# Kernel optimization log

Hardware: AMD Instinct MI355X
Metric: run time of the kernel (lower is better)

Reference implementation:

```python
import jax, jax.numpy as jnp
import numpy as np
from jax import lax

B = 128
NODES = 304
T_STEPS = 20
HID = 64
GCN_IN = 20
N = B * NODES            # 38912 graph nodes
E = N * 16               # 622592 edges
BN_EPS = 1e-5


def setup_inputs() -> dict:
    key = jax.random.key(0)
    ks = jax.random.split(key, 32)
    rn = lambda k, s, sc=0.1: jax.random.normal(k, s, jnp.float32) * sc
    return {
        "data_x": jax.random.normal(ks[0], (N, GCN_IN), jnp.float32),
        "edge_index": jax.random.randint(ks[1], (2, E), 0, N),
        "edge_weight": jax.random.uniform(ks[2], (E,), jnp.float32),
        "tc1_w1": rn(ks[3], (HID, 1, 1, 3)), "tc1_b1": rn(ks[4], (HID,)),
        "tc1_w2": rn(ks[5], (HID, 1, 1, 3)), "tc1_b2": rn(ks[6], (HID,)),
        "tc1_w3": rn(ks[7], (HID, 1, 1, 3)), "tc1_b3": rn(ks[8], (HID,)),
        "gcn_W0": rn(ks[9], (GCN_IN, HID)), "gcn_b0": rn(ks[10], (HID,)),
        "bn0_g": jax.random.uniform(ks[11], (HID,), jnp.float32, 0.5, 1.5), "bn0_b": rn(ks[12], (HID,)),
        "gcn_W1": rn(ks[13], (HID, HID)), "gcn_b1": rn(ks[14], (HID,)),
        "bn1_g": jax.random.uniform(ks[15], (HID,), jnp.float32, 0.5, 1.5), "bn1_b": rn(ks[16], (HID,)),
        "tc2_w1": rn(ks[17], (1, HID, 1, 3)), "tc2_b1": rn(ks[18], (1,)),
        "tc2_w2": rn(ks[19], (1, HID, 1, 3)), "tc2_b2": rn(ks[20], (1,)),
        "tc2_w3": rn(ks[21], (1, HID, 1, 3)), "tc2_b3": rn(ks[22], (1,)),
        "bn2d_g": jax.random.uniform(ks[23], (NODES,), jnp.float32, 0.5, 1.5), "bn2d_b": rn(ks[24], (NODES,)),
        "fc_W": rn(ks[25], (21 * NODES, 2048), 0.01), "fc_b": rn(ks[26], (2048,)),
        "fc4_W": rn(ks[27], (2048, 300), 0.01), "fc4_b": rn(ks[28], (300,)),
    }


def _bn(x, g, b):
    # eval-mode BatchNorm with fresh running stats (mean=0, var=1)
    return x * (g / jnp.sqrt(1.0 + BN_EPS)) + b


def _temporal_conv(X, w1, b1, w2, b2, w3, b3):
    # X: [B, T, nodes, C] -> permute to NCHW [B, C, nodes, T]
    Xp = jnp.transpose(X, (0, 3, 2, 1))
    conv = lambda w, b: lax.conv_general_dilated(
        Xp, w, (1, 1), [(0, 0), (1, 1)],
        dimension_numbers=("NCHW", "OIHW", "NCHW")) + b[None, :, None, None]
    P = conv(w1, b1)
    Q = jax.nn.sigmoid(conv(w2, b2))
    H = jax.nn.relu(P * Q + conv(w3, b3))
    return jnp.transpose(H, (0, 3, 2, 1))  # back to [B, T, nodes, C_out]


def reference(data_x, edge_index, edge_weight,
              tc1_w1, tc1_b1, tc1_w2, tc1_b2, tc1_w3, tc1_b3,
              gcn_W0, gcn_b0, bn0_g, bn0_b,
              gcn_W1, gcn_b1, bn1_g, bn1_b,
              tc2_w1, tc2_b1, tc2_w2, tc2_b2, tc2_w3, tc2_b3,
              bn2d_g, bn2d_b, fc_W, fc_b, fc4_W, fc4_b):
    n = data_x.shape[0]
    b = n // NODES

    # ---- GCN norm (sym, self-loops w=1) ----
    row, col = edge_index[0], edge_index[1]
    loop = jnp.arange(n)
    rowF = jnp.concatenate([row, loop])
    colF = jnp.concatenate([col, loop])
    ewF = jnp.concatenate([edge_weight, jnp.ones((n,), data_x.dtype)])
    deg = jax.ops.segment_sum(ewF, colF, num_segments=n)
    dinv = lax.rsqrt(jnp.maximum(deg, 1e-12))
    norm = dinv[rowF] * ewF * dinv[colF]

    def gconv(x, W, bias):
        h = x @ W
        return jax.ops.segment_sum(h[rowF] * norm[:, None], colF, num_segments=n) + bias

    x = jax.nn.relu(_bn(gconv(data_x, gcn_W0, gcn_b0), bn0_g, bn0_b))
    x = jax.nn.relu(_bn(gconv(x, gcn_W1, gcn_b1), bn1_g, bn1_b))  # [N, HID]

    # ---- temporal conv 1 ----
    X = data_x.reshape(b, T_STEPS, NODES, 1)
    T0 = _temporal_conv(X, tc1_w1, tc1_b1, tc1_w2, tc1_b2, tc1_w3, tc1_b3)  # [B,20,304,HID]

    # gcn_feature.permute(1,0).reshape(-1, 1, nodes, HID)
    gfeat = x.T.reshape(b, 1, NODES, HID)

    T = jnp.concatenate([jax.nn.relu(T0), gfeat], axis=1)  # [B, 21, 304, HID]
    T = jax.nn.relu(T)

    # ---- temporal conv 2 ----
    T = _temporal_conv(T, tc2_w1, tc2_b1, tc2_w2, tc2_b2, tc2_w3, tc2_b3)  # [B,21,304,1]

    # BatchNorm2d over node channel (axis=2 here), eval-mode running stats
    T = T * (bn2d_g / jnp.sqrt(1.0 + BN_EPS))[None, None, :, None] + bn2d_b[None, None, :, None]

    T = T.reshape(b, -1)  # [B, 6384]
    T = jax.nn.relu(T @ fc_W + fc_b)
    return T @ fc4_W + fc4_b  # [B, 300]
```

## Files before the change

### kernel.cpp

```cpp
#include <hip/hip_runtime.h>

#define NODES   304
#define BATCH   128
#define TSTEPS  20
#define HID     64
#define GCNIN   20
#define NN      (BATCH*NODES)
#define NE      (NN*16)
#define SEGSZ   (NN/4)
#define BCAP    64
#define FC1_IN  (21*NODES)
#define KP1     6400
#define FC1_OUT 2048
#define FC2_OUT 300
#define NP2     304
#define BN_EPS  1e-5f

typedef __attribute__((ext_vector_type(8))) short short8;
typedef __attribute__((ext_vector_type(4))) float f32x4;
typedef __attribute__((ext_vector_type(2))) float f32x2;

static __device__ __forceinline__ short f2bf(float x) {
    unsigned u = __float_as_uint(x);
    unsigned r = (u + 0x7FFF + ((u >> 16) & 1)) >> 16;
    return (short)r;
}
static __device__ __forceinline__ float bf2f(unsigned short v) {
    return __uint_as_float((unsigned)v << 16);
}

static __device__ __forceinline__ float fast_sigmoid(float q) {
    return __builtin_amdgcn_rcpf(1.f + __expf(-q));
}

static __device__ __forceinline__ f32x2 pk_fma(f32x2 a, f32x2 b, f32x2 c) {
    f32x2 d;
    asm("v_pk_fma_f32 %0, %1, %2, %3" : "=v"(d) : "v"(a), "v"(b), "v"(c));
    return d;
}

template <int C>
static __device__ __forceinline__ float dppadd(float v) {
    return v + __int_as_float(
        __builtin_amdgcn_update_dpp(0, __float_as_int(v), C, 0xF, 0xF, false));
}
static __device__ __forceinline__ float rsum16(float v) {
    v = dppadd<0x128>(v);
    v = dppadd<0x124>(v);
    v = dppadd<0x122>(v);
    v = dppadd<0x121>(v);
    return v;
}

__global__ void k_bucket(const int* __restrict__ ei, const float* __restrict__ ew,
                         int* __restrict__ cnt, int2* __restrict__ bucket) {
    int e = blockIdx.x * blockDim.x + threadIdx.x;
    if (e < NE) {
        int c = ei[NE + e];
        int slot = atomicAdd(&cnt[c], 1);
        if (slot < BCAP) {
            int2 v;
            v.x = ei[e];
            v.y = __float_as_int(ew[e]);
            bucket[((size_t)c << 6) + slot] = v;
        }
    }
}

__global__ __launch_bounds__(256) void k_cvtX(const float* __restrict__ X,
                                              const int* __restrict__ cnt,
                                              const int2* __restrict__ bucket,
                                              unsigned short* __restrict__ Xb,
                                              float* __restrict__ dinv) {
    int wv = threadIdx.x >> 5, f = threadIdx.x & 31;
    int n = blockIdx.x * 8 + wv;
    __shared__ float rs[8][2];

    int2 e0 = bucket[((size_t)n << 6) + f];
    int2 e1 = bucket[((size_t)n << 6) + 32 + f];
    int deg = cnt[n];
    float xv = (f < GCNIN) ? X[(size_t)n * GCNIN + f] : 0.f;

    int dcap = deg < BCAP ? deg : BCAP;
    float s = ((f < dcap) ? __int_as_float(e0.y) : 0.f) +
              ((32 + f < dcap) ? __int_as_float(e1.y) : 0.f);
    s = rsum16(s);
    if ((f & 15) == 0) rs[wv][f >> 4] = s;
    __syncthreads();

    float dv = rsqrtf(fmaxf(1.f + rs[wv][0] + rs[wv][1], 1e-12f));
    if (f == 0) dinv[n] = dv;
    Xb[(size_t)n * 32 + f] = (f < GCNIN) ? (unsigned short)f2bf(xv * dv)
                                         : (unsigned short)0;
}

static __device__ __forceinline__ void stage_partition(
    int deg, int2 e, int f, int wv, int (*sIdx)[BCAP], float (*sWt)[BCAP],
    int& dcap) {
    dcap = deg < BCAP ? deg : BCAP;
    bool valid = f < dcap;
    int row = e.x;
    float w = __int_as_float(e.y);
    int q = (row >= SEGSZ) + (row >= 2 * SEGSZ) + (row >= 3 * SEGSZ);
    unsigned long long b0 = __ballot(valid && q == 0);
    unsigned long long b1 = __ballot(valid && q == 1);
    unsigned long long b2 = __ballot(valid && q == 2);
    unsigned long long b3 = __ballot(valid && q == 3);
    unsigned long long lmask = (1ULL << f) - 1;
    int pos = 0;
    if (q > 0) pos += __popcll(b0);
    if (q > 1) pos += __popcll(b1);
    if (q > 2) pos += __popcll(b2);
    unsigned long long mybal = (q == 0) ? b0 : (q == 1) ? b1 : (q == 2) ? b2 : b3;
    pos += __popcll(mybal & lmask);
    if (valid) {
        sIdx[wv][pos] = row;
        sWt[wv][pos] = w;
    }
}

__global__ __launch_bounds__(256) void k_gather20(const int* __restrict__ cnt,
                                                  const int2* __restrict__ bucket,
                                                  const float* __restrict__ dinv,
                                                  const unsigned short* __restrict__ Xb,
                                                  const float* __restrict__ W0,
                                                  const float* __restrict__ gb,
                                                  const float* __restrict__ bng,
                                                  const float* __restrict__ bnb,
                                                  const float* __restrict__ W1,
                                                  unsigned short* __restrict__ H1) {
    int wv = threadIdx.x >> 6, f = threadIdx.x & 63;
    int c = blockIdx.x * 4 + wv;
    int g = f >> 4, r = f & 15;
    __shared__ int sIdx[4][BCAP];
    __shared__ float sWt[4][BCAP];
    __shared__ float agg[4][32];
    __shared__ float xs[4][HID];

    int2 be = bucket[((size_t)c << 6) + f];
    int deg = cnt[c];
    float dc = dinv[c];
    unsigned selfv = *(const unsigned*)(Xb + (size_t)c * 32 + 2 * r);

    int dcap;
    stage_partition(deg, be, f, wv, sIdx, sWt, dcap);
    __syncthreads();

    f32x2 acc2;
    acc2[0] = 0.f;
    acc2[1] = 0.f;
    for (int base = 0; base < dcap; base += 16) {
        int idx[4];
        float w[4];
#pragma unroll
        for (int i = 0; i < 4; i++) {
            int l = base + (i << 2) + g;
            int lc = (l < dcap) ? l : dcap - 1;
            idx[i] = sIdx[wv][lc];
            w[i] = (l < dcap) ? sWt[wv][lc] : 0.f;
        }
        unsigned vv[4];
#pragma unroll
        for (int i = 0; i < 4; i++)
            vv[i] = *(const unsigned*)(Xb + (size_t)idx[i] * 32 + 2 * r);
#pragma unroll
        for (int i = 0; i < 4; i++) {
            acc2[0] = fmaf(bf2f((unsigned short)(vv[i] & 0xffff)), w[i], acc2[0]);
            acc2[1] = fmaf(bf2f((unsigned short)(vv[i] >> 16)), w[i], acc2[1]);
        }
    }
    acc2[0] += __shfl_xor(acc2[0], 16);
    acc2[0] += __shfl_xor(acc2[0], 32);
    acc2[1] += __shfl_xor(acc2[1], 16);
    acc2[1] += __shfl_xor(acc2[1], 32);
    if (g == 0) {
        agg[wv][2 * r] = acc2[0] + bf2f((unsigned short)(selfv & 0xffff));
        agg[wv][2 * r + 1] = acc2[1] + bf2f((unsigned short)(selfv >> 16));
    }
    __syncthreads();

    float v = 0.f;
#pragma unroll
    for (int k = 0; k < GCNIN; k++) v = fmaf(agg[wv][k], W0[k * HID + f], v);
    float scale = bng[f] * rsqrtf(1.f + BN_EPS);
    float y = fmaxf(fmaf(v * dc + gb[f], scale, bnb[f]), 0.f);

    xs[wv][f] = y;
    __syncthreads();
    float h = 0.f;
#pragma unroll
    for (int k4 = 0; k4 < HID / 4; k4++) {
        float4 xv = *(const float4*)&xs[wv][k4 * 4];
        h = fmaf(xv.x, W1[(k4 * 4 + 0) * HID + f], h);
        h = fmaf(xv.y, W1[(k4 * 4 + 1) * HID + f], h);
        h = fmaf(xv.z, W1[(k4 * 4 + 2) * HID + f], h);
        h = fmaf(xv.w, W1[(k4 * 4 + 3) * HID + f], h);
    }
    H1[(size_t)c * HID + f] = (unsigned short)f2bf(h * dc);
}

__global__ __launch_bounds__(256) void k_gatherB(const int* __restrict__ cnt,
                                                 const int2* __restrict__ bucket,
                                                 const float* __restrict__ dinv,
                                                 const unsigned short* __restrict__ H,
                                                 const float* __restrict__ gb,
                                                 const float* __restrict__ bng,
                                                 const float* __restrict__ bnb,
                                                 float* __restrict__ XO) {
    int wv = threadIdx.x >> 6, f = threadIdx.x & 63;
    int c = blockIdx.x * 4 + wv;
    int g = f >> 4, r = f & 15;
    __shared__ int sIdx[4][BCAP];
    __shared__ float sWt[4][BCAP];

    int2 be = bucket[((size_t)c << 6) + f];
    int deg = cnt[c];
    float dc = dinv[c];
    ushort4 selfv = *(const ushort4*)(H + (size_t)c * HID + 4 * r);

    int dcap;
    stage_partition(deg, be, f, wv, sIdx, sWt, dcap);
    __syncthreads();

    float a0 = 0.f, a1 = 0.f, a2 = 0.f, a3 = 0.f;
    for (int base = 0; base < dcap; base += 16) {
        int idx[4];
        float w[4];
#pragma unroll
        for (int i = 0; i < 4; i++) {
            int l = base + (i << 2) + g;
            int lc = (l < dcap) ? l : dcap - 1;
            idx[i] = sIdx[wv][lc];
            w[i] = (l < dcap) ? sWt[wv][lc] : 0.f;
        }
        ushort4 hv[4];
#pragma unroll
        for (int i = 0; i < 4; i++)
            hv[i] = *(const ushort4*)(H + (size_t)idx[i] * HID + 4 * r);
#pragma unroll
        for (int i = 0; i < 4; i++) {
            a0 = fmaf(bf2f(hv[i].x), w[i], a0);
            a1 = fmaf(bf2f(hv[i].y), w[i], a1);
            a2 = fmaf(bf2f(hv[i].z), w[i], a2);
            a3 = fmaf(bf2f(hv[i].w), w[i], a3);
        }
    }
    a0 += __shfl_xor(a0, 16); a0 += __shfl_xor(a0, 32);
    a1 += __shfl_xor(a1, 16); a1 += __shfl_xor(a1, 32);
    a2 += __shfl_xor(a2, 16); a2 += __shfl_xor(a2, 32);
    a3 += __shfl_xor(a3, 16); a3 += __shfl_xor(a3, 32);

    if (g == 0) {
        float4 scv = *(const float4*)&bng[4 * r];
        float4 bbv = *(const float4*)&bnb[4 * r];
        float4 gbv = *(const float4*)&gb[4 * r];
        float rr = rsqrtf(1.f + BN_EPS);
        float4 o;
        o.x = fmaxf(fmaf((a0 + bf2f(selfv.x)) * dc + gbv.x, scv.x * rr, bbv.x), 0.f);
        o.y = fmaxf(fmaf((a1 + bf2f(selfv.y)) * dc + gbv.y, scv.y * rr, bbv.y), 0.f);
        o.z = fmaxf(fmaf((a2 + bf2f(selfv.z)) * dc + gbv.z, scv.z * rr, bbv.z), 0.f);
        o.w = fmaxf(fmaf((a3 + bf2f(selfv.w)) * dc + gbv.w, scv.w * rr, bbv.w), 0.f);
        *(float4*)(XO + (size_t)c * HID + 4 * r) = o;
    }
}

__global__ __launch_bounds__(256) void k_xpose(const float* __restrict__ x2,
                                               float* __restrict__ x2t) {
    __shared__ float tile[64][65];
    int n0 = blockIdx.x * 64;
    for (int i = threadIdx.x; i < 4096; i += 256) {
        int r = i >> 6, h = i & 63;
        tile[r][h] = x2[(size_t)(n0 + r) * 64 + h];
    }
    __syncthreads();
    for (int i = threadIdx.x; i < 4096; i += 256) {
        int h = i >> 6, c = i & 63;
        x2t[(size_t)h * NN + n0 + c] = tile[c][h];
    }
}

static __device__ __forceinline__ void load12(const float* base, f32x2 P[2][3]) {
    float4 f0 = *(const float4*)(base);
    float4 f1 = *(const float4*)(base + 4);
    float4 f2 = *(const float4*)(base + 8);
    P[0][0][0] = f0.x; P[0][0][1] = f0.w;
    P[0][1][0] = f0.y; P[0][1][1] = f1.x;
    P[0][2][0] = f0.z; P[0][2][1] = f1.y;
    P[1][0][0] = f1.z; P[1][0][1] = f2.y;
    P[1][1][0] = f1.w; P[1][1][1] = f2.z;
    P[1][2][0] = f2.x; P[1][2][1] = f2.w;
}

__global__ __launch_bounds__(256) void k_temporal2(
    const float* __restrict__ data_x, const float* __restrict__ x2t,
    const float* __restrict__ w1, const float* __restrict__ b1,
    const float* __restrict__ w2, const float* __restrict__ b2,
    const float* __restrict__ w3, const float* __restrict__ b3,
    const float* __restrict__ v1, const float* __restrict__ vb1,
    const float* __restrict__ v2, const float* __restrict__ vb2,
    const float* __restrict__ v3, const float* __restrict__ vb3,
    const float* __restrict__ bn2g, const float* __restrict__ bn2b,
    short* __restrict__ Ab) {
    int bn0 = blockIdx.x * 16;
    int b = bn0 / NODES, node0 = bn0 % NODES;
    int tid = threadIdx.x;
    int p = tid >> 4;
    int c0 = (tid & 15) << 2;
    int node = node0 + p;

    __shared__ float xs[16][22];
    __shared__ float wlds[1344];

    if (tid < 192) {
        wlds[tid] = w1[tid];
        wlds[192 + tid] = w2[tid];
        wlds[384 + tid] = w3[tid];
        wlds[576 + tid] = v1[tid];
        wlds[768 + tid] = v2[tid];
        wlds[960 + tid] = v3[tid];
    }
    if (tid < 64) {
        wlds[1152 + tid] = b1[tid];
        wlds[1216 + tid] = b2[tid];
        wlds[1280 + tid] = b3[tid];
    }
    for (int i = tid; i < 320; i += 256) {
        int t = i >> 4, pp = i & 15;
        xs[pp][t + 1] = data_x[b * (TSTEPS * NODES) + t * NODES + node0 + pp];
    }
    if (tid < 16) { xs[tid][0] = 0.f; xs[tid][21] = 0.f; }

    float cb1 = vb1[0], cb2 = vb2[0], cb3 = vb3[0];
    float s2 = bn2g[node] * rsqrtf(1.f + BN_EPS);
    float bb2 = bn2b[node];
    short* dst = Ab + (size_t)b * KP1;

    __syncthreads();

    f32x2 A1p[2][3], A2p[2][3], A3p[2][3], B1p[2], B2p[2], B3p[2];
    f32x2 U1p[2][3], U2p[2][3], U3p[2][3];
    load12(&wlds[0 + c0 * 3], A1p);
    load12(&wlds[192 + c0 * 3], A2p);
    load12(&wlds[384 + c0 * 3], A3p);
    load12(&wlds[576 + c0 * 3], U1p);
    load12(&wlds[768 + c0 * 3], U2p);
    load12(&wlds[960 + c0 * 3], U3p);
    {
        float4 t1 = *(const float4*)&wlds[1152 + c0];
        float4 t2 = *(const float4*)&wlds[1216 + c0];
        float4 t3 = *(const float4*)&wlds[1280 + c0];
        B1p[0][0] = t1.x; B1p[0][1] = t1.y; B1p[1][0] = t1.z; B1p[1][1] = t1.w;
        B2p[0][0] = t2.x; B2p[0][1] = t2.y; B2p[1][0] = t2.z; B2p[1][1] = t2.w;
        B3p[0][0] = t3.x; B3p[0][1] = t3.y; B3p[1][0] = t3.z; B3p[1][1] = t3.w;
    }

    f32x2 hA2[2] = {}, hB2[2] = {}, hC2[2];
    float xr0 = xs[p][0], xr1 = xs[p][1];

#pragma unroll
    for (int j = 0; j <= 21; j++) {
        if (j < 20) {
            float xr2 = xs[p][j + 2];
            f32x2 x0d, x1d, x2d;
            x0d[0] = xr0; x0d[1] = xr0;
            x1d[0] = xr1; x1d[1] = xr1;
            x2d[0] = xr2; x2d[1] = xr2;
#pragma unroll
            for (int cp = 0; cp < 2; cp++) {
                f32x2 pv = pk_fma(A1p[cp][2], x2d,
                            pk_fma(A1p[cp][1], x1d, pk_fma(A1p[cp][0], x0d, B1p[cp])));
                f32x2 qv = pk_fma(A2p[cp][2], x2d,
                            pk_fma(A2p[cp][1], x1d, pk_fma(A2p[cp][0], x0d, B2p[cp])));
                f32x2 rv = pk_fma(A3p[cp][2], x2d,
                            pk_fma(A3p[cp][1], x1d, pk_fma(A3p[cp][0], x0d, B3p[cp])));
                hC2[cp][0] = fmaxf(fmaf(pv[0], fast_sigmoid(qv[0]), rv[0]), 0.f);
                hC2[cp][1] = fmaxf(fmaf(pv[1], fast_sigmoid(qv[1]), rv[1]), 0.f);
            }
            xr0 = xr1;
            xr1 = xr2;
        } else if (j == 20) {
            const float4 gv = *(const float4*)(x2t + (size_t)(b >> 1) * NN +
                                               (b & 1) * (NODES * HID) + node * HID + c0);
            hC2[0][0] = fmaxf(gv.x, 0.f);
            hC2[0][1] = fmaxf(gv.y, 0.f);
            hC2[1][0] = fmaxf(gv.z, 0.f);
            hC2[1][1] = fmaxf(gv.w, 0.f);
        } else {
            hC2[0][0] = 0.f; hC2[0][1] = 0.f;
            hC2[1][0] = 0.f; hC2[1][1] = 0.f;
        }
        if (j >= 1) {
            int w = j - 1;
            f32x2 pa, qa, ra;
            pa[0] = 0.f; pa[1] = 0.f;
            qa[0] = 0.f; qa[1] = 0.f;
            ra[0] = 0.f; ra[1] = 0.f;
#pragma unroll
            for (int cp = 0; cp < 2; cp++) {
                pa = pk_fma(U1p[cp][0], hA2[cp], pa);
                pa = pk_fma(U1p[cp][1], hB2[cp], pa);
                pa = pk_fma(U1p[cp][2], hC2[cp], pa);
                qa = pk_fma(U2p[cp][0], hA2[cp], qa);
                qa = pk_fma(U2p[cp][1], hB2[cp], qa);
                qa = pk_fma(U2p[cp][2], hC2[cp], qa);
                ra = pk_fma(U3p[cp][0], hA2[cp], ra);
                ra = pk_fma(U3p[cp][1], hB2[cp], ra);
                ra = pk_fma(U3p[cp][2], hC2[cp], ra);
            }
            float pp_ = rsum16(pa[0] + pa[1]);
            float qq_ = rsum16(qa[0] + qa[1]);
            float rr_ = rsum16(ra[0] + ra[1]);
            float P = pp_ + cb1, Q = qq_ + cb2, R = rr_ + cb3;
            float hv = fmaxf(fmaf(P, fast_sigmoid(Q), R), 0.f);
            if ((tid & 15) == 0) dst[w * NODES + node] = f2bf(fmaf(hv, s2, bb2));
        }
        hA2[0] = hB2[0]; hA2[1] = hB2[1];
        hB2[0] = hC2[0]; hB2[1] = hC2[1];
    }
}

__global__ __launch_bounds__(256) void k_cvtW4(const float* __restrict__ W,
                                               short* __restrict__ Wt) {
    __shared__ float t[32][33];
    int tx = threadIdx.x & 31, ty = threadIdx.x >> 5;
    int n0 = blockIdx.x * 32, k0 = blockIdx.y * 32;
#pragma unroll
    for (int r = 0; r < 32; r += 8) {
        int k = k0 + r + ty, n = n0 + tx;
        t[r + ty][tx] = (n < FC2_OUT) ? W[(size_t)k * FC2_OUT + n] : 0.f;
    }
    __syncthreads();
#pragma unroll
    for (int r = 0; r < 32; r += 8) {
        int n = n0 + r + ty;
        if (n < NP2) Wt[(size_t)n * FC1_OUT + k0 + tx] = f2bf(t[tx][r + ty]);
    }
}

#define KSPL1 8
#define KCH1  (KP1 / KSPL1)
__global__ __launch_bounds__(256) void k_gemm1f(const short* __restrict__ Ab,
                                                const float* __restrict__ fcW,
                                                float* __restrict__ part) {
    int lane = threadIdx.x & 63, wv = threadIdx.x >> 6;
    int r = lane & 15, kg = lane >> 4;
    int nb = blockIdx.x * 64, sp = blockIdx.y;

    f32x4 acc[2][4] = {};
    const short* a0 = Ab + (size_t)(wv * 32 + r) * KP1;
    const short* a1 = a0 + (size_t)16 * KP1;

    int k0 = sp * KCH1 + kg * 8;
    const float* wp = fcW + (size_t)k0 * FC1_OUT + nb + r;
    bool tailblk = (sp == KSPL1 - 1);

#pragma unroll 1
    for (int s = 0; s < KCH1 / 32; s++, k0 += 32) {
        short8 av0 = *(const short8*)(a0 + k0);
        short8 av1 = *(const short8*)(a1 + k0);
        short8 bv[4];
        if (tailblk && s == KCH1 / 32 - 1) {
#pragma unroll
            for (int f = 0; f < 4; f++)
#pragma unroll
                for (int i = 0; i < 8; i++) {
                    float v = (k0 + i < FC1_IN) ? wp[(size_t)i * FC1_OUT + f * 16] : 0.f;
                    bv[f][i] = f2bf(v);
                }
        } else {
#pragma unroll
            for (int f = 0; f < 4; f++)
#pragma unroll
                for (int i = 0; i < 8; i++)
                    bv[f][i] = f2bf(wp[(size_t)i * FC1_OUT + f * 16]);
        }
        acc[0][0] = __builtin_amdgcn_mfma_f32_16x16x32_bf16(av0, bv[0], acc[0][0], 0, 0, 0);
        acc[1][0] = __builtin_amdgcn_mfma_f32_16x16x32_bf16(av1, bv[0], acc[1][0], 0, 0, 0);
        acc[0][1] = __builtin_amdgcn_mfma_f32_16x16x32_bf16(av0, bv[1], acc[0][1], 0, 0, 0);
        acc[1][1] = __builtin_amdgcn_mfma_f32_16x16x32_bf16(av1, bv[1], acc[1][1], 0, 0, 0);
        acc[0][2] = __builtin_amdgcn_mfma_f32_16x16x32_bf16(av0, bv[2], acc[0][2], 0, 0, 0);
        acc[1][2] = __builtin_amdgcn_mfma_f32_16x16x32_bf16(av1, bv[2], acc[1][2], 0, 0, 0);
        acc[0][3] = __builtin_amdgcn_mfma_f32_16x16x32_bf16(av0, bv[3], acc[0][3], 0, 0, 0);
        acc[1][3] = __builtin_amdgcn_mfma_f32_16x16x32_bf16(av1, bv[3], acc[1][3], 0, 0, 0);
        wp += (size_t)32 * FC1_OUT;
    }

    float* dst = part + (size_t)sp * BATCH * FC1_OUT;
#pragma unroll
    for (int m = 0; m < 2; m++)
#pragma unroll
        for (int f = 0; f < 4; f++)
#pragma unroll
            for (int j = 0; j < 4; j++) {
                int row = wv * 32 + m * 16 + kg * 4 + j;
                int col = nb + f * 16 + r;
                dst[(size_t)row * FC1_OUT + col] = acc[m][f][j];
            }
}

__global__ __launch_bounds__(256) void k_reduce1(const float* __restrict__ part,
                                                 const float* __restrict__ bias,
                                                 short* __restrict__ Ab2) {
    int idx = blockIdx.x * 256 + threadIdx.x;
    int o = idx & (FC1_OUT - 1);
    float s = bias[o];
#pragma unroll
    for (int sp = 0; sp < KSPL1; sp++) s += part[(size_t)sp * BATCH * FC1_OUT + idx];
    Ab2[idx] = f2bf(fmaxf(s, 0.f));
}

#define KSPL2 8
#define KCH2  (FC1_OUT / KSPL2)
__global__ __launch_bounds__(256) void k_gemm2(const short* __restrict__ Ab,
                                               const short* __restrict__ Wt,
                                               float* __restrict__ part) {
    int lane = threadIdx.x & 63, wv = threadIdx.x >> 6;
    int r = lane & 15, kg = lane >> 4;
    int nb = blockIdx.x * 16, sp = blockIdx.y;

    f32x4 acc[2] = {};
    const short* a0 = Ab + (size_t)(wv * 32 + r) * FC1_OUT;
    const short* a1 = a0 + (size_t)16 * FC1_OUT;
    const short* bp = Wt + (size_t)(nb + r) * FC1_OUT;

    int k0 = sp * KCH2 + kg * 8;
#pragma unroll
    for (int s = 0; s < KCH2 / 32; s++, k0 += 32) {
        short8 av0 = *(const short8*)(a0 + k0);
        short8 av1 = *(const short8*)(a1 + k0);
        short8 bv = *(const short8*)(bp + k0);
        acc[0] = __builtin_amdgcn_mfma_f32_16x16x32_bf16(av0, bv, acc[0], 0, 0, 0);
        acc[1] = __builtin_amdgcn_mfma_f32_16x16x32_bf16(av1, bv, acc[1], 0, 0, 0);
    }

    float* dst = part + (size_t)sp * BATCH * NP2;
#pragma unroll
    for (int m = 0; m < 2; m++)
#pragma unroll
        for (int j = 0; j < 4; j++) {
            int row = wv * 32 + m * 16 + kg * 4 + j;
            int col = nb + r;
            dst[(size_t)row * NP2 + col] = acc[m][j];
        }
}

__global__ __launch_bounds__(256) void k_reduce2(const float* __restrict__ part,
                                                 const float* __restrict__ bias,
                                                 float* __restrict__ out) {
    int idx = blockIdx.x * 256 + threadIdx.x;
    if (idx >= BATCH * NP2) return;
    int b = idx / NP2, o = idx % NP2;
    float s = 0.f;
#pragma unroll
    for (int sp = 0; sp < KSPL2; sp++) s += part[(size_t)sp * BATCH * NP2 + idx];
    if (o < FC2_OUT) out[(size_t)b * FC2_OUT + o] = s + bias[o];
}

extern "C" void kernel_launch(void* const* d_in, const int* in_sizes, int n_in,
                              void* d_out, int out_size, void* d_ws, size_t ws_size,
                              hipStream_t stream) {
    const float* data_x = (const float*)d_in[0];
    const int* ei = (const int*)d_in[1];
    const float* ew = (const float*)d_in[2];
    const float* tc1w1 = (const float*)d_in[3];
    const float* tc1b1 = (const float*)d_in[4];
    const float* tc1w2 = (const float*)d_in[5];
    const float* tc1b2 = (const float*)d_in[6];
    const float* tc1w3 = (const float*)d_in[7];
    const float* tc1b3 = (const float*)d_in[8];
    const float* W0 = (const float*)d_in[9];
    const float* gb0 = (const float*)d_in[10];
    const float* bn0g = (const float*)d_in[11];
    const float* bn0b = (const float*)d_in[12];
    const float* W1 = (const float*)d_in[13];
    const float* gb1 = (const float*)d_in[14];
    const float* bn1g = (const float*)d_in[15];
    const float* bn1b = (const float*)d_in[16];
    const float* tc2w1 = (const float*)d_in[17];
    const float* tc2b1 = (const float*)d_in[18];
    const float* tc2w2 = (const float*)d_in[19];
    const float* tc2b2 = (const float*)d_in[20];
    const float* tc2w3 = (const float*)d_in[21];
    const float* tc2b3 = (const float*)d_in[22];
    const float* bn2g = (const float*)d_in[23];
    const float* bn2b = (const float*)d_in[24];
    const float* fcW = (const float*)d_in[25];
    const float* fcb = (const float*)d_in[26];
    const float* fc4W = (const float*)d_in[27];
    const float* fc4b = (const float*)d_in[28];
    float* out = (float*)d_out;

    char* ws = (char*)d_ws;
    float* x2 = (float*)(ws + 0);
    short* Ab = (short*)(ws + 9961472);
    const size_t ARENA = 9961472 + 1638400;

    size_t off = ARENA;
    auto alloc = [&](size_t bytes) -> void* {
        void* p = ws + off;
        off = (off + bytes + 255) & ~(size_t)255;
        return p;
    };
    int2* bucket = (int2*)alloc((size_t)NN * BCAP * 8);
    int* cnt = (int*)alloc((size_t)NN * 4);
    float* dinv = (float*)alloc((size_t)NN * 4);
    unsigned short* Xb = (unsigned short*)alloc((size_t)NN * 32 * 2);
    unsigned short* h1 = (unsigned short*)alloc((size_t)NN * HID * 2);

    float* x2t = (float*)(ws + ARENA);

    off = ARENA;
    float* part1 = (float*)alloc((size_t)KSPL1 * BATCH * FC1_OUT * 4);
    short* Ab2 = (short*)alloc((size_t)BATCH * FC1_OUT * 2);
    short* W4t = (short*)alloc((size_t)NP2 * FC1_OUT * 2);
    float* part2 = (float*)alloc((size_t)KSPL2 * BATCH * NP2 * 4);
    (void)ws_size; (void)in_sizes; (void)n_in; (void)out_size;

    hipMemsetAsync(cnt, 0, (size_t)NN * 4, stream);
    k_bucket<<<(NE + 255) / 256, 256, 0, stream>>>(ei, ew, cnt, bucket);

    k_cvtX<<<NN / 8, 256, 0, stream>>>(data_x, cnt, bucket, Xb, dinv);
    k_gather20<<<NN / 4, 256, 0, stream>>>(cnt, bucket, dinv, Xb, W0, gb0, bn0g,
                                           bn0b, W1, h1);
    k_gatherB<<<NN / 4, 256, 0, stream>>>(cnt, bucket, dinv, h1, gb1, bn1g, bn1b, x2);

    k_xpose<<<NN / 64, 256, 0, stream>>>(x2, x2t);

    hipMemsetAsync(Ab, 0, (size_t)BATCH * KP1 * 2, stream);
    k_temporal2<<<NN / 16, 256, 0, stream>>>(data_x, x2t, tc1w1, tc1b1, tc1w2, tc1b2,
                                             tc1w3, tc1b3, tc2w1, tc2b1, tc2w2, tc2b2,
                                             tc2w3, tc2b3, bn2g, bn2b, Ab);

    {
        dim3 g(FC1_OUT / 64, KSPL1);
        k_gemm1f<<<g, 256, 0, stream>>>(Ab, fcW, part1);
    }
    k_reduce1<<<BATCH * FC1_OUT / 256, 256, 0, stream>>>(part1, fcb, Ab2);
    {
        dim3 g((NP2 + 31) / 32, FC1_OUT / 32);
        k_cvtW4<<<g, 256, 0, stream>>>(fc4W, W4t);
    }
    {
        dim3 g(NP2 / 16, KSPL2);
        k_gemm2<<<g, 256, 0, stream>>>(Ab2, W4t, part2);
    }
    k_reduce2<<<(BATCH * NP2 + 255) / 256, 256, 0, stream>>>(part2, fc4b, out);
}
```

Measured before the change: 190.7 us.

## Split GCN gather by channel halves, restructure temporal conv, fuse fc4 weight conversion

The second GCN gather is split into two launches, each handling 32 channels with 4-byte loads, to shrink each gathered footprint and improve cache hit rates. The temporal kernel now computes all 21 first-stage outputs into a register array before running the second conv, replacing the rolling three-slot window. The separate fc4 weight transpose/convert kernel is removed, and gemm2 now reads fp32 weights directly with strided loads and converts them inline. Risks include doubled gather launch overhead and index reads, higher register pressure in the temporal kernel, and uncoalesced weight reads in gemm2.

```diff
diff --git a/kernel.cpp b/kernel.cpp
--- a/kernel.cpp
+++ b/kernel.cpp
@@ -199,30 +199,32 @@
     H1[(size_t)c * HID + f] = (unsigned short)f2bf(h * dc);
 }
 
-__global__ __launch_bounds__(256) void k_gatherB(const int* __restrict__ cnt,
-                                                 const int2* __restrict__ bucket,
-                                                 const float* __restrict__ dinv,
-                                                 const unsigned short* __restrict__ H,
-                                                 const float* __restrict__ gb,
-                                                 const float* __restrict__ bng,
-                                                 const float* __restrict__ bnb,
-                                                 float* __restrict__ XO) {
+template <int HALF>
+__global__ __launch_bounds__(256) void k_gatherBh(const int* __restrict__ cnt,
+                                                  const int2* __restrict__ bucket,
+                                                  const float* __restrict__ dinv,
+                                                  const unsigned short* __restrict__ H,
+                                                  const float* __restrict__ gb,
+                                                  const float* __restrict__ bng,
+                                                  const float* __restrict__ bnb,
+                                                  float* __restrict__ XO) {
     int wv = threadIdx.x >> 6, f = threadIdx.x & 63;
     int c = blockIdx.x * 4 + wv;
     int g = f >> 4, r = f & 15;
+    int ch = HALF * 32 + 2 * r;
     __shared__ int sIdx[4][BCAP];
     __shared__ float sWt[4][BCAP];
 
     int2 be = bucket[((size_t)c << 6) + f];
     int deg = cnt[c];
     float dc = dinv[c];
-    ushort4 selfv = *(const ushort4*)(H + (size_t)c * HID + 4 * r);
+    unsigned selfv = *(const unsigned*)(H + (size_t)c * HID + ch);
 
     int dcap;
     stage_partition(deg, be, f, wv, sIdx, sWt, dcap);
     __syncthreads();
 
-    float a0 = 0.f, a1 = 0.f, a2 = 0.f, a3 = 0.f;
+    float a0 = 0.f, a1 = 0.f;
     for (int base = 0; base < dcap; base += 16) {
         int idx[4];
         float w[4];
@@ -233,34 +235,29 @@
             idx[i] = sIdx[wv][lc];
             w[i] = (l < dcap) ? sWt[wv][lc] : 0.f;
         }
-        ushort4 hv[4];
+        unsigned hv[4];
 #pragma unroll
         for (int i = 0; i < 4; i++)
-            hv[i] = *(const ushort4*)(H + (size_t)idx[i] * HID + 4 * r);
+            hv[i] = *(const unsigned*)(H + (size_t)idx[i] * HID + ch);
 #pragma unroll
         for (int i = 0; i < 4; i++) {
-            a0 = fmaf(bf2f(hv[i].x), w[i], a0);
-            a1 = fmaf(bf2f(hv[i].y), w[i], a1);
-            a2 = fmaf(bf2f(hv[i].z), w[i], a2);
-            a3 = fmaf(bf2f(hv[i].w), w[i], a3);
-        }
-    }
-    a0 += __shfl_xor(a0, 16); a0 += __shfl_xor(a0, 32);
-    a1 += __shfl_xor(a1, 16); a1 += __shfl_xor(a1, 32);
-    a2 += __shfl_xor(a2, 16); a2 += __shfl_xor(a2, 32);
-    a3 += __shfl_xor(a3, 16); a3 += __shfl_xor(a3, 32);
+            a0 = fmaf(bf2f((unsigned short)(hv[i] & 0xffff)), w[i], a0);
+            a1 = fmaf(bf2f((unsigned short)(hv[i] >> 16)), w[i], a1);
+        }
+    }
+    a0 += __shfl_xor(a0, 16);
+    a0 += __shfl_xor(a0, 32);
+    a1 += __shfl_xor(a1, 16);
+    a1 += __shfl_xor(a1, 32);
 
     if (g == 0) {
-        float4 scv = *(const float4*)&bng[4 * r];
-        float4 bbv = *(const float4*)&bnb[4 * r];
-        float4 gbv = *(const float4*)&gb[4 * r];
         float rr = rsqrtf(1.f + BN_EPS);
-        float4 o;
-        o.x = fmaxf(fmaf((a0 + bf2f(selfv.x)) * dc + gbv.x, scv.x * rr, bbv.x), 0.f);
-        o.y = fmaxf(fmaf((a1 + bf2f(selfv.y)) * dc + gbv.y, scv.y * rr, bbv.y), 0.f);
-        o.z = fmaxf(fmaf((a2 + bf2f(selfv.z)) * dc + gbv.z, scv.z * rr, bbv.z), 0.f);
-        o.w = fmaxf(fmaf((a3 + bf2f(selfv.w)) * dc + gbv.w, scv.w * rr, bbv.w), 0.f);
-        *(float4*)(XO + (size_t)c * HID + 4 * r) = o;
+        float2 o;
+        o.x = fmaxf(fmaf((a0 + bf2f((unsigned short)(selfv & 0xffff))) * dc + gb[ch],
+                         bng[ch] * rr, bnb[ch]), 0.f);
+        o.y = fmaxf(fmaf((a1 + bf2f((unsigned short)(selfv >> 16))) * dc + gb[ch + 1],
+                         bng[ch + 1] * rr, bnb[ch + 1]), 0.f);
+        *(float2*)(XO + (size_t)c * HID + ch) = o;
     }
 }
 
@@ -291,7 +288,7 @@
     P[1][2][0] = f2.x; P[1][2][1] = f2.w;
 }
 
-__global__ __launch_bounds__(256) void k_temporal2(
+__global__ __launch_bounds__(256) void k_temporal3(
     const float* __restrict__ data_x, const float* __restrict__ x2t,
     const float* __restrict__ w1, const float* __restrict__ b1,
     const float* __restrict__ w2, const float* __restrict__ b2,
@@ -337,103 +334,84 @@
 
     __syncthreads();
 
-    f32x2 A1p[2][3], A2p[2][3], A3p[2][3], B1p[2], B2p[2], B3p[2];
+    f32x2 h[21][2];
+    {
+        f32x2 A1p[2][3], A2p[2][3], A3p[2][3], B1p[2], B2p[2], B3p[2];
+        load12(&wlds[0 + c0 * 3], A1p);
+        load12(&wlds[192 + c0 * 3], A2p);
+        load12(&wlds[384 + c0 * 3], A3p);
+        {
+            float4 t1 = *(const float4*)&wlds[1152 + c0];
+            float4 t2 = *(const float4*)&wlds[1216 + c0];
+            float4 t3 = *(const float4*)&wlds[1280 + c0];
+            B1p[0][0] = t1.x; B1p[0][1] = t1.y; B1p[1][0] = t1.z; B1p[1][1] = t1.w;
+            B2p[0][0] = t2.x; B2p[0][1] = t2.y; B2p[1][0] = t2.z; B2p[1][1] = t2.w;
+            B3p[0][0] = t3.x; B3p[0][1] = t3.y; B3p[1][0] = t3.z; B3p[1][1] = t3.w;
+        }
+        f32x2 xp0, xp1;
+        xp0[0] = xs[p][0]; xp0[1] = xs[p][0];
+        xp1[0] = xs[p][1]; xp1[1] = xs[p][1];
+#pragma unroll
+        for (int t = 0; t < TSTEPS; t++) {
+            float x2s = xs[p][t + 2];
+            f32x2 xp2;
+            xp2[0] = x2s; xp2[1] = x2s;
+#pragma unroll
+            for (int cp = 0; cp < 2; cp++) {
+                f32x2 pv = pk_fma(A1p[cp][2], xp2,
+                            pk_fma(A1p[cp][1], xp1, pk_fma(A1p[cp][0], xp0, B1p[cp])));
+                f32x2 qv = pk_fma(A2p[cp][2], xp2,
+                            pk_fma(A2p[cp][1], xp1, pk_fma(A2p[cp][0], xp0, B2p[cp])));
+                f32x2 rv = pk_fma(A3p[cp][2], xp2,
+                            pk_fma(A3p[cp][1], xp1, pk_fma(A3p[cp][0], xp0, B3p[cp])));
+                h[t][cp][0] = fmaxf(fmaf(pv[0], fast_sigmoid(qv[0]), rv[0]), 0.f);
+                h[t][cp][1] = fmaxf(fmaf(pv[1], fast_sigmoid(qv[1]), rv[1]), 0.f);
+            }
+            xp0 = xp1;
+            xp1 = xp2;
+        }
+    }
+    {
+        const float4 gv = *(const float4*)(x2t + (size_t)(b >> 1) * NN +
+                                           (b & 1) * (NODES * HID) + node * HID + c0);
+        h[20][0][0] = fmaxf(gv.x, 0.f);
+        h[20][0][1] = fmaxf(gv.y, 0.f);
+        h[20][1][0] = fmaxf(gv.z, 0.f);
+        h[20][1][1] = fmaxf(gv.w, 0.f);
+    }
+
     f32x2 U1p[2][3], U2p[2][3], U3p[2][3];
-    load12(&wlds[0 + c0 * 3], A1p);
-    load12(&wlds[192 + c0 * 3], A2p);
-    load12(&wlds[384 + c0 * 3], A3p);
     load12(&wlds[576 + c0 * 3], U1p);
     load12(&wlds[768 + c0 * 3], U2p);
     load12(&wlds[960 + c0 * 3], U3p);
-    {
-        float4 t1 = *(const float4*)&wlds[1152 + c0];
-        float4 t2 = *(const float4*)&wlds[1216 + c0];
-        float4 t3 = *(const float4*)&wlds[1280 + c0];
-        B1p[0][0] = t1.x; B1p[0][1] = t1.y; B1p[1][0] = t1.z; B1p[1][1] = t1.w;
-        B2p[0][0] = t2.x; B2p[0][1] = t2.y; B2p[1][0] = t2.z; B2p[1][1] = t2.w;
-        B3p[0][0] = t3.x; B3p[0][1] = t3.y; B3p[1][0] = t3.z; B3p[1][1] = t3.w;
-    }
-
-    f32x2 hA2[2] = {}, hB2[2] = {}, hC2[2];
-    float xr0 = xs[p][0], xr1 = xs[p][1];
-
-#pragma unroll
-    for (int j = 0; j <= 21; j++) {
-        if (j < 20) {
-            float xr2 = xs[p][j + 2];
-            f32x2 x0d, x1d, x2d;
-            x0d[0] = xr0; x0d[1] = xr0;
-            x1d[0] = xr1; x1d[1] = xr1;
-            x2d[0] = xr2; x2d[1] = xr2;
-#pragma unroll
-            for (int cp = 0; cp < 2; cp++) {
-                f32x2 pv = pk_fma(A1p[cp][2], x2d,
-                            pk_fma(A1p[cp][1], x1d, pk_fma(A1p[cp][0], x0d, B1p[cp])));
-                f32x2 qv = pk_fma(A2p[cp][2], x2d,
-                            pk_fma(A2p[cp][1], x1d, pk_fma(A2p[cp][0], x0d, B2p[cp])));
-                f32x2 rv = pk_fma(A3p[cp][2], x2d,
-                            pk_fma(A3p[cp][1], x1d, pk_fma(A3p[cp][0], x0d, B3p[cp])));
-                hC2[cp][0] = fmaxf(fmaf(pv[0], fast_sigmoid(qv[0]), rv[0]), 0.f);
-                hC2[cp][1] = fmaxf(fmaf(pv[1], fast_sigmoid(qv[1]), rv[1]), 0.f);
-            }
-            xr0 = xr1;
-            xr1 = xr2;
-        } else if (j == 20) {
-            const float4 gv = *(const float4*)(x2t + (size_t)(b >> 1) * NN +
-                                               (b & 1) * (NODES * HID) + node * HID + c0);
-            hC2[0][0] = fmaxf(gv.x, 0.f);
-            hC2[0][1] = fmaxf(gv.y, 0.f);
-            hC2[1][0] = fmaxf(gv.z, 0.f);
-            hC2[1][1] = fmaxf(gv.w, 0.f);
-        } else {
-            hC2[0][0] = 0.f; hC2[0][1] = 0.f;
-            hC2[1][0] = 0.f; hC2[1][1] = 0.f;
-        }
-        if (j >= 1) {
-            int w = j - 1;
-            f32x2 pa, qa, ra;
-            pa[0] = 0.f; pa[1] = 0.f;
-            qa[0] = 0.f; qa[1] = 0.f;
-            ra[0] = 0.f; ra[1] = 0.f;
-#pragma unroll
-            for (int cp = 0; cp < 2; cp++) {
-                pa = pk_fma(U1p[cp][0], hA2[cp], pa);
-                pa = pk_fma(U1p[cp][1], hB2[cp], pa);
-                pa = pk_fma(U1p[cp][2], hC2[cp], pa);
-                qa = pk_fma(U2p[cp][0], hA2[cp], qa);
-                qa = pk_fma(U2p[cp][1], hB2[cp], qa);
-                qa = pk_fma(U2p[cp][2], hC2[cp], qa);
-                ra = pk_fma(U3p[cp][0], hA2[cp], ra);
-                ra = pk_fma(U3p[cp][1], hB2[cp], ra);
-                ra = pk_fma(U3p[cp][2], hC2[cp], ra);
-            }
-            float pp_ = rsum16(pa[0] + pa[1]);
-            float qq_ = rsum16(qa[0] + qa[1]);
-            float rr_ = rsum16(ra[0] + ra[1]);
-            float P = pp_ + cb1, Q = qq_ + cb2, R = rr_ + cb3;
-            float hv = fmaxf(fmaf(P, fast_sigmoid(Q), R), 0.f);
-            if ((tid & 15) == 0) dst[w * NODES + node] = f2bf(fmaf(hv, s2, bb2));
-        }
-        hA2[0] = hB2[0]; hA2[1] = hB2[1];
-        hB2[0] = hC2[0]; hB2[1] = hC2[1];
-    }
-}
-
-__global__ __launch_bounds__(256) void k_cvtW4(const float* __restrict__ W,
-                                               short* __restrict__ Wt) {
-    __shared__ float t[32][33];
-    int tx = threadIdx.x & 31, ty = threadIdx.x >> 5;
-    int n0 = blockIdx.x * 32, k0 = blockIdx.y * 32;
-#pragma unroll
-    for (int r = 0; r < 32; r += 8) {
-        int k = k0 + r + ty, n = n0 + tx;
-        t[r + ty][tx] = (n < FC2_OUT) ? W[(size_t)k * FC2_OUT + n] : 0.f;
-    }
-    __syncthreads();
-#pragma unroll
-    for (int r = 0; r < 32; r += 8) {
-        int n = n0 + r + ty;
-        if (n < NP2) Wt[(size_t)n * FC1_OUT + k0 + tx] = f2bf(t[tx][r + ty]);
+    f32x2 zero2;
+    zero2[0] = 0.f;
+    zero2[1] = 0.f;
+
+#pragma unroll
+    for (int w = 0; w < 21; w++) {
+        f32x2 pa = zero2, qa = zero2, ra = zero2;
+#pragma unroll
+        for (int cp = 0; cp < 2; cp++) {
+            f32x2 hm = (w == 0) ? zero2 : h[w - 1][cp];
+            f32x2 h0 = h[w][cp];
+            f32x2 hp = (w == 20) ? zero2 : h[w + 1][cp];
+            pa = pk_fma(U1p[cp][0], hm, pa);
+            pa = pk_fma(U1p[cp][1], h0, pa);
+            pa = pk_fma(U1p[cp][2], hp, pa);
+            qa = pk_fma(U2p[cp][0], hm, qa);
+            qa = pk_fma(U2p[cp][1], h0, qa);
+            qa = pk_fma(U2p[cp][2], hp, qa);
+            ra = pk_fma(U3p[cp][0], hm, ra);
+            ra = pk_fma(U3p[cp][1], h0, ra);
+            ra = pk_fma(U3p[cp][2], hp, ra);
+        }
+        float pp_ = rsum16(pa[0] + pa[1]);
+        float qq_ = rsum16(qa[0] + qa[1]);
+        float rr_ = rsum16(ra[0] + ra[1]);
+        float P = pp_ + cb1, Q = qq_ + cb2, R = rr_ + cb3;
+        float hv = fmaxf(fmaf(P, fast_sigmoid(Q), R), 0.f);
+        if ((tid & 15) == 0) dst[w * NODES + node] = f2bf(fmaf(hv, s2, bb2));
     }
 }
 
@@ -511,9 +489,9 @@
 
 #define KSPL2 8
 #define KCH2  (FC1_OUT / KSPL2)
-__global__ __launch_bounds__(256) void k_gemm2(const short* __restrict__ Ab,
-                                               const short* __restrict__ Wt,
-                                               float* __restrict__ part) {
+__global__ __launch_bounds__(256) void k_gemm2f(const short* __restrict__ Ab,
+                                                const float* __restrict__ fc4W,
+                                                float* __restrict__ part) {
     int lane = threadIdx.x & 63, wv = threadIdx.x >> 6;
     int r = lane & 15, kg = lane >> 4;
     int nb = blockIdx.x * 16, sp = blockIdx.y;
@@ -521,16 +499,21 @@
     f32x4 acc[2] = {};
     const short* a0 = Ab + (size_t)(wv * 32 + r) * FC1_OUT;
     const short* a1 = a0 + (size_t)16 * FC1_OUT;
-    const short* bp = Wt + (size_t)(nb + r) * FC1_OUT;
+    int col = nb + r;
+    int colc = (col < FC2_OUT) ? col : FC2_OUT - 1;
 
     int k0 = sp * KCH2 + kg * 8;
-#pragma unroll
+    const float* wp = fc4W + (size_t)k0 * FC2_OUT + colc;
+#pragma unroll 1
     for (int s = 0; s < KCH2 / 32; s++, k0 += 32) {
         short8 av0 = *(const short8*)(a0 + k0);
         short8 av1 = *(const short8*)(a1 + k0);
-        short8 bv = *(const short8*)(bp + k0);
+        short8 bv;
+#pragma unroll
+        for (int i = 0; i < 8; i++) bv[i] = f2bf(wp[(size_t)i * FC2_OUT]);
         acc[0] = __builtin_amdgcn_mfma_f32_16x16x32_bf16(av0, bv, acc[0], 0, 0, 0);
         acc[1] = __builtin_amdgcn_mfma_f32_16x16x32_bf16(av1, bv, acc[1], 0, 0, 0);
+        wp += (size_t)32 * FC2_OUT;
     }
 
     float* dst = part + (size_t)sp * BATCH * NP2;
@@ -539,7 +522,6 @@
 #pragma unroll
         for (int j = 0; j < 4; j++) {
             int row = wv * 32 + m * 16 + kg * 4 + j;
-            int col = nb + r;
             dst[(size_t)row * NP2 + col] = acc[m][j];
         }
 }
@@ -612,7 +594,6 @@
     off = ARENA;
     float* part1 = (float*)alloc((size_t)KSPL1 * BATCH * FC1_OUT * 4);
     short* Ab2 = (short*)alloc((size_t)BATCH * FC1_OUT * 2);
-    short* W4t = (short*)alloc((size_t)NP2 * FC1_OUT * 2);
     float* part2 = (float*)alloc((size_t)KSPL2 * BATCH * NP2 * 4);
     (void)ws_size; (void)in_sizes; (void)n_in; (void)out_size;
 
@@ -622,12 +603,15 @@
     k_cvtX<<<NN / 8, 256, 0, stream>>>(data_x, cnt, bucket, Xb, dinv);
     k_gather20<<<NN / 4, 256, 0, stream>>>(cnt, bucket, dinv, Xb, W0, gb0, bn0g,
                                            bn0b, W1, h1);
-    k_gatherB<<<NN / 4, 256, 0, stream>>>(cnt, bucket, dinv, h1, gb1, bn1g, bn1b, x2);
+    k_gatherBh<0><<<NN / 4, 256, 0, stream>>>(cnt, bucket, dinv, h1, gb1, bn1g,
+                                              bn1b, x2);
+    k_gatherBh<1><<<NN / 4, 256, 0, stream>>>(cnt, bucket, dinv, h1, gb1, bn1g,
+                                              bn1b, x2);
 
     k_xpose<<<NN / 64, 256, 0, stream>>>(x2, x2t);
 
     hipMemsetAsync(Ab, 0, (size_t)BATCH * KP1 * 2, stream);
-    k_temporal2<<<NN / 16, 256, 0, stream>>>(data_x, x2t, tc1w1, tc1b1, tc1w2, tc1b2,
+    k_temporal3<<<NN / 16, 256, 0, stream>>>(data_x, x2t, tc1w1, tc1b1, tc1w2, tc1b2,
                                              tc1w3, tc1b3, tc2w1, tc2b1, tc2w2, tc2b2,
                                              tc2w3, tc2b3, bn2g, bn2b, Ab);
 
@@ -637,12 +621,8 @@
     }
     k_reduce1<<<BATCH * FC1_OUT / 256, 256, 0, stream>>>(part1, fcb, Ab2);
     {
-        dim3 g((NP2 + 31) / 32, FC1_OUT / 32);
-        k_cvtW4<<<g, 256, 0, stream>>>(fc4W, W4t);
-    }
-    {
         dim3 g(NP2 / 16, KSPL2);
-        k_gemm2<<<g, 256, 0, stream>>>(Ab2, W4t, part2);
+        k_gemm2f<<<g, 256, 0, stream>>>(Ab2, fc4W, part2);
     }
     k_reduce2<<<(BATCH * NP2 + 255) / 256, 256, 0, stream>>>(part2, fc4b, out);
 }
```

Result: slower. 229.0 us (+20.1%).
